# Kernel tuning notes

Measured on AMD Instinct MI355X. Metric: run time of the kernel, lower is better.

## Reference

```python
import jax, jax.numpy as jnp
import numpy as np

BS, D_NUM, SLEN, DIM = 64, 2, 50, 64   # batch, domains, history len, embedding_dim
NUM_EMB = 512                          # codebook size (hardcoded in source)
NEG_INF = -1e30                        # stand-in for -np.inf (NaN-safe under softmax grad)


def setup_inputs() -> dict:
    key = jax.random.key(0)
    ks = jax.random.split(key, 16)
    w = lambda k, shape: jax.random.normal(k, shape, jnp.float32) * 0.05
    inp = {
        "x": jax.random.normal(ks[0], (BS, D_NUM, SLEN, DIM), jnp.float32),
        "code_book": jax.random.normal(ks[1], (NUM_EMB, DIM), jnp.float32) * 0.1,
        "Wq_is": w(ks[2], (DIM, DIM)), "bq_is": jnp.zeros((DIM,), jnp.float32),
        "Wk_is": w(ks[3], (DIM, DIM)), "bk_is": jnp.zeros((DIM,), jnp.float32),
        "Wv_is": w(ks[4], (DIM, DIM)), "bv_is": jnp.zeros((DIM,), jnp.float32),
        "Wq_cs": w(ks[5], (DIM, DIM)), "bq_cs": jnp.zeros((DIM,), jnp.float32),
        "Wk_cs": w(ks[6], (DIM, DIM)), "bk_cs": jnp.zeros((DIM,), jnp.float32),
        "Wv_cs": w(ks[7], (DIM, DIM)), "bv_cs": jnp.zeros((DIM,), jnp.float32),
    }
    return inp


def reference(x, code_book,
              Wq_is, bq_is, Wk_is, bk_is, Wv_is, bv_is,
              Wq_cs, bq_cs, Wk_cs, bk_cs, Wv_cs, bv_cs):
    bs, dn, sl, dim = x.shape
    flat = x.reshape(-1, dim)  # [N, dim], N = bs*dn*sl

    # ---- get_quantized: cdist + argmin + codebook lookup ----
    # ||f||^2 + ||c||^2 - 2 f c^T, argmin over codebook, gather (== one_hot @ code_book)
    dists = (jnp.sum(flat * flat, axis=1, keepdims=True)
             + jnp.sum(code_book * code_book, axis=1)
             - 2.0 * flat @ code_book.T)                      # [N, NUM_EMB]
    idx = jnp.argmin(dists, axis=1)                           # [N]
    quantized = code_book[idx].reshape(x.shape)               # [bs, dn, sl, dim]

    # ---- intra-sample (IS) attention: softmax(K Q^T) V per (sample, domain) ----
    q = (flat @ Wq_is + bq_is).reshape(bs, dn, sl, dim)
    k = (flat @ Wk_is + bk_is).reshape(bs, dn, sl, dim)
    v = (flat @ Wv_is + bv_is).reshape(bs, dn, sl, dim)
    is_kq = jnp.einsum('bdse,bdte->bdst', k, q)               # K @ Q^T, [bs, dn, sl, sl]
    Z = jnp.einsum('bdst,bdte->bdse', jax.nn.softmax(is_kq, axis=-1), v)

    # ---- cross-sample (CS) attention: dense NxN, own-sample block masked out ----
    qc = flat @ Wq_cs + bq_cs                                  # [N, dim]
    kc = flat @ Wk_cs + bk_cs
    vc = flat @ Wv_cs + bv_cs
    sid = jnp.repeat(jnp.arange(bs), dn * sl)                  # sample id per row
    same = sid[:, None] == sid[None, :]                        # block-diagonal mask
    scores = kc @ qc.T                                         # [N, N]
    scores = jnp.where(same, NEG_INF, scores)                  # mask own-sample block
    X = (jax.nn.softmax(scores, axis=-1) @ vc).reshape(x.shape)

    return quantized, Z, X
```

## Files before the change

### kernel.cpp

```cpp
#include <hip/hip_runtime.h>
#include <hip/hip_bf16.h>
#include <math.h>

#define DIM 64
#define NROW 6400
#define SLEN 50
#define NG 128
#define NEMB 512
#define SAMPLE 100
#define NCHUNK 100
#define NQB 400
#define SMAX 6
#define LOG2E 1.4426950408889634f
#define SM_SHIFT2 11.541560327111707f
#define LSTR 72

typedef unsigned short ushort_t;
typedef __attribute__((ext_vector_type(8))) short short8;
typedef __attribute__((ext_vector_type(4))) float floatx4;

__device__ __forceinline__ ushort_t f2bu(float f) {
    __hip_bfloat16 h = __float2bfloat16(f);
    ushort_t u;
    __builtin_memcpy(&u, &h, 2);
    return u;
}

__device__ __forceinline__ float fast_exp2(float x) {
#if __has_builtin(__builtin_amdgcn_exp2f)
    return __builtin_amdgcn_exp2f(x);
#else
    return exp2f(x);
#endif
}

__global__ __launch_bounds__(64)
void prep_kernel(const float* __restrict__ W0, const float* __restrict__ W1,
                 const float* __restrict__ W2, const float* __restrict__ W3,
                 const float* __restrict__ W4, const float* __restrict__ W5,
                 ushort_t* __restrict__ Wt,
                 const float* __restrict__ cb, float* __restrict__ cbT,
                 double* __restrict__ c2)
{
    if (blockIdx.x < 6) {
        const float* Ws[6] = {W0, W1, W2, W3, W4, W5};
        const int p = blockIdx.x;
        const int n = threadIdx.x;
        const float* W = Ws[p];
        const float scale = (p == 1 || p == 4) ? LOG2E : 1.0f;
        ushort_t* dst = Wt + (size_t)p * DIM * DIM + (size_t)n * DIM;
#pragma unroll 8
        for (int k = 0; k < DIM; ++k)
            dst[k] = f2bu(W[(size_t)k * DIM + n] * scale);
    } else {
        const int c = (blockIdx.x - 6) * 64 + threadIdx.x;
        const float* cr = cb + (size_t)c * DIM;
        double s = 0.0;
#pragma unroll 8
        for (int e = 0; e < DIM; ++e) {
            const float v = cr[e];
            cbT[(size_t)e * NEMB + c] = v;
            s = fma((double)v, (double)v, s);
        }
        c2[c] = s;
    }
}

__global__ __launch_bounds__(256)
void proj_kernel(const float* __restrict__ x, const ushort_t* __restrict__ Wt,
                 const float* __restrict__ b0, const float* __restrict__ b1,
                 const float* __restrict__ b2, const float* __restrict__ b3,
                 const float* __restrict__ b4, const float* __restrict__ b5,
                 ushort_t* __restrict__ qib, ushort_t* __restrict__ kib,
                 ushort_t* __restrict__ vib,
                 ushort_t* __restrict__ qcb, ushort_t* __restrict__ kcb,
                 ushort_t* __restrict__ vtb)
{
    __shared__ __align__(16) ushort_t Xb[64 * LSTR];

    const int tid = threadIdx.x;
    const int wave = tid >> 6, lane = tid & 63;
    const int col = lane & 15;
    const int quad = lane >> 4;

    const int r0 = (blockIdx.x >> 1) * 64;
    const int pbase = (blockIdx.x & 1) * 3;

    {
        const int r = tid >> 2, seg = tid & 3;
        const float* src = x + (size_t)(r0 + r) * DIM + seg * 16;
        ushort_t* dst = &Xb[r * LSTR + seg * 16];
#pragma unroll
        for (int i = 0; i < 16; ++i) dst[i] = f2bu(src[i]);
    }
    __syncthreads();

    const short8 aX0 = *(const short8*)&Xb[(wave * 16 + col) * LSTR + quad * 8];
    const short8 aX1 = *(const short8*)&Xb[(wave * 16 + col) * LSTR + quad * 8 + 32];

    const float* Bs[6] = {b0, b1, b2, b3, b4, b5};
#pragma unroll
    for (int pp = 0; pp < 3; ++pp) {
        const int p = pbase + pp;
        const ushort_t* Wtp = Wt + (size_t)p * DIM * DIM;
#pragma unroll
        for (int nt = 0; nt < 4; ++nt) {
            const int n = nt * 16 + col;
            float bv = Bs[p][n];
            if (p == 1 || p == 4) bv *= LOG2E;
            floatx4 c = (floatx4){bv, bv, bv, bv};
            const ushort_t* wr = Wtp + (size_t)n * DIM + quad * 8;
            const short8 w0 = *(const short8*)wr;
            const short8 w1 = *(const short8*)(wr + 32);
            c = __builtin_amdgcn_mfma_f32_16x16x32_bf16(aX0, w0, c, 0, 0, 0);
            c = __builtin_amdgcn_mfma_f32_16x16x32_bf16(aX1, w1, c, 0, 0, 0);
#pragma unroll
            for (int r = 0; r < 4; ++r) {
                const int row = r0 + wave * 16 + quad * 4 + r;
                const ushort_t ub = f2bu(c[r]);
                if (p == 0)      qib[(size_t)row * DIM + n] = ub;
                else if (p == 1) kib[(size_t)row * DIM + n] = ub;
                else if (p == 2) vib[(size_t)row * DIM + n] = ub;
                else if (p == 3) qcb[(size_t)row * DIM + n] = ub;
                else if (p == 4) kcb[(size_t)row * DIM + n] = ub;
                else             vtb[(size_t)n * NROW + row] = ub;
            }
        }
    }
}

__global__ __launch_bounds__(256, 5)
void attn_quant_kernel(const ushort_t* __restrict__ qib, const ushort_t* __restrict__ kib,
                       const ushort_t* __restrict__ vib, float* __restrict__ outZ,
                       const ushort_t* __restrict__ qcb, const ushort_t* __restrict__ kcb,
                       const ushort_t* __restrict__ vtb,
                       float* __restrict__ pl, float* __restrict__ pacc,
                       float* __restrict__ outX,
                       const float* __restrict__ x, const float* __restrict__ cb,
                       const float* __restrict__ cbT, const double* __restrict__ c2,
                       float* __restrict__ outq,
                       int S, int direct)
{
    __shared__ __align__(16) ushort_t smem[3 * 64 * LSTR];

    const int tid = threadIdx.x;
    const int wave = tid >> 6;
    const int lane = tid & 63;

    if ((int)blockIdx.x < NQB) {
        const int r0 = blockIdx.x * 16;

        double* xs    = (double*)smem;
        double* f2s   = xs + 16 * 64;
        double* candd = f2s + 16;
        int*    candi = (int*)(candd + 64);
        int*    sidx  = candi + 64;

        for (int idx = tid; idx < 16 * DIM; idx += 256) {
            const int r = idx >> 6, e = idx & 63;
            xs[r * 64 + e] = (double)x[(size_t)(r0 + r) * DIM + e];
        }
        __syncthreads();
        if (tid < 16) {
            double s = 0.0;
#pragma unroll 8
            for (int e = 0; e < DIM; ++e) s = fma(xs[tid * 64 + e], xs[tid * 64 + e], s);
            f2s[tid] = s;
        }
        __syncthreads();

        const int c0 = wave * 64 + lane;
        double dot0[16], dot1[16];
#pragma unroll
        for (int r = 0; r < 16; ++r) { dot0[r] = 0.0; dot1[r] = 0.0; }

        for (int e = 0; e < DIM; ++e) {
            const double ce0 = (double)cbT[(size_t)e * NEMB + c0];
            const double ce1 = (double)cbT[(size_t)e * NEMB + c0 + 256];
#pragma unroll
            for (int r = 0; r < 16; ++r) {
                const double xe = xs[r * 64 + e];
                dot0[r] = fma(xe, ce0, dot0[r]);
                dot1[r] = fma(xe, ce1, dot1[r]);
            }
        }

#pragma unroll
        for (int r = 0; r < 16; ++r) {
            const double f2r = f2s[r];
            double bd = f2r + c2[c0] - 2.0 * dot0[r];
            int bi = c0;
            const double d1 = f2r + c2[c0 + 256] - 2.0 * dot1[r];
            if (d1 < bd) { bd = d1; bi = c0 + 256; }
            for (int off = 32; off; off >>= 1) {
                const double od = __shfl_down(bd, off, 64);
                const int oi = __shfl_down(bi, off, 64);
                if (od < bd || (od == bd && oi < bi)) { bd = od; bi = oi; }
            }
            if (lane == 0) { candd[wave * 16 + r] = bd; candi[wave * 16 + r] = bi; }
        }
        __syncthreads();
        if (tid < 16) {
            double bd = candd[tid];
            int bi = candi[tid];
#pragma unroll
            for (int w = 1; w < 4; ++w) {
                const double od = candd[w * 16 + tid];
                const int oi = candi[w * 16 + tid];
                if (od < bd || (od == bd && oi < bi)) { bd = od; bi = oi; }
            }
            sidx[tid] = bi;
        }
        __syncthreads();
        for (int idx = tid; idx < 16 * DIM; idx += 256) {
            const int r = idx >> 6, e = idx & 63;
            outq[(size_t)(r0 + r) * DIM + e] = cb[(size_t)sidx[r] * DIM + e];
        }
        return;
    }

    const int ab = blockIdx.x - NQB;
    const int col = lane & 15;
    const int quad = lane >> 4;

    short8 ones;
#pragma unroll
    for (int i = 0; i < 8; ++i) ones[i] = (short)0x3F80;

    if (ab < 100 * S) {
        const int bi = ab / S;
        const int split = ab % S;
        const int i0 = bi * 64 + wave * 16;

        ushort_t* Qs = smem;
        ushort_t* Vs = smem + 64 * LSTR;
        ushort_t* Pb = smem + 2 * 64 * LSTR + wave * 16 * LSTR;

        const int srow = tid >> 2;
        const int sseg = tid & 3;

        short8 aK0, aK1;
        {
            const ushort_t* kr = kcb + (size_t)(i0 + col) * DIM + quad * 8;
            aK0 = *(const short8*)kr;
            aK1 = *(const short8*)(kr + 32);
        }

        int lo[4];
        float l[4];
        floatx4 O[4];
#pragma unroll
        for (int r = 0; r < 4; ++r) {
            lo[r] = ((i0 + quad * 4 + r) / SAMPLE) * SAMPLE;
            l[r] = 0.f;
        }
#pragma unroll
        for (int et = 0; et < 4; ++et) O[et] = (floatx4){0.f, 0.f, 0.f, 0.f};

        {
            const int j0 = split * 64;
            const uint4* qsrc = (const uint4*)(qcb + (size_t)(j0 + srow) * DIM + sseg * 16);
            const uint4* vsrc = (const uint4*)(vtb + (size_t)srow * NROW + j0 + sseg * 16);
            const uint4 q0 = qsrc[0], q1 = qsrc[1];
            const uint4 v0 = vsrc[0], v1 = vsrc[1];
            uint4* qdst = (uint4*)&Qs[srow * LSTR + sseg * 16];
            uint4* vdst = (uint4*)&Vs[srow * LSTR + sseg * 16];
            qdst[0] = q0; qdst[1] = q1;
            vdst[0] = v0; vdst[1] = v1;
        }
        __syncthreads();

        for (int ch = split; ch < NCHUNK; ch += S) {
            const int nxt = ch + S;
            uint4 q0, q1, v0, v1;
            if (nxt < NCHUNK) {
                const int j0n = nxt * 64;
                const uint4* qsrc = (const uint4*)(qcb + (size_t)(j0n + srow) * DIM + sseg * 16);
                const uint4* vsrc = (const uint4*)(vtb + (size_t)srow * NROW + j0n + sseg * 16);
                q0 = qsrc[0]; q1 = qsrc[1];
                v0 = vsrc[0]; v1 = vsrc[1];
            }

            const int j0 = ch * 64;

            floatx4 Sv[4];
#pragma unroll
            for (int jt = 0; jt < 4; ++jt) {
                const short8 b0 = *(const short8*)&Qs[(jt * 16 + col) * LSTR + quad * 8];
                const short8 b1 = *(const short8*)&Qs[(jt * 16 + col) * LSTR + quad * 8 + 32];
                floatx4 c = (floatx4){0.f, 0.f, 0.f, 0.f};
                c = __builtin_amdgcn_mfma_f32_16x16x32_bf16(aK0, b0, c, 0, 0, 0);
                c = __builtin_amdgcn_mfma_f32_16x16x32_bf16(aK1, b1, c, 0, 0, 0);
                Sv[jt] = c;
            }

#pragma unroll
            for (int jt = 0; jt < 4; ++jt) {
                const int jj = j0 + jt * 16 + col;
#pragma unroll
                for (int r = 0; r < 4; ++r) {
                    float p = fast_exp2(Sv[jt][r] - SM_SHIFT2);
                    if ((unsigned)(jj - lo[r]) < SAMPLE) p = 0.f;
                    Pb[(quad * 4 + r) * LSTR + jt * 16 + col] = f2bu(p);
                }
            }

            const short8 aP0 = *(const short8*)&Pb[col * LSTR + quad * 8];
            const short8 aP1 = *(const short8*)&Pb[col * LSTR + quad * 8 + 32];

            floatx4 rsv = (floatx4){0.f, 0.f, 0.f, 0.f};
            rsv = __builtin_amdgcn_mfma_f32_16x16x32_bf16(aP0, ones, rsv, 0, 0, 0);
            rsv = __builtin_amdgcn_mfma_f32_16x16x32_bf16(aP1, ones, rsv, 0, 0, 0);
#pragma unroll
            for (int r = 0; r < 4; ++r) l[r] += rsv[r];

#pragma unroll
            for (int et = 0; et < 4; ++et) {
                const short8 b0 = *(const short8*)&Vs[(et * 16 + col) * LSTR + quad * 8];
                const short8 b1 = *(const short8*)&Vs[(et * 16 + col) * LSTR + quad * 8 + 32];
                O[et] = __builtin_amdgcn_mfma_f32_16x16x32_bf16(aP0, b0, O[et], 0, 0, 0);
                O[et] = __builtin_amdgcn_mfma_f32_16x16x32_bf16(aP1, b1, O[et], 0, 0, 0);
            }

            if (nxt < NCHUNK) {
                __syncthreads();
                uint4* qdst = (uint4*)&Qs[srow * LSTR + sseg * 16];
                uint4* vdst = (uint4*)&Vs[srow * LSTR + sseg * 16];
                qdst[0] = q0; qdst[1] = q1;
                vdst[0] = v0; vdst[1] = v1;
                __syncthreads();
            }
        }

        if (direct) {
#pragma unroll
            for (int et = 0; et < 4; ++et)
#pragma unroll
                for (int r = 0; r < 4; ++r)
                    outX[(size_t)(i0 + quad * 4 + r) * DIM + et * 16 + col] = O[et][r] / l[r];
        } else {
#pragma unroll
            for (int et = 0; et < 4; ++et)
#pragma unroll
                for (int r = 0; r < 4; ++r)
                    pacc[((size_t)split * NROW + i0 + quad * 4 + r) * DIM + et * 16 + col] = O[et][r];
            if (col == 0) {
#pragma unroll
                for (int r = 0; r < 4; ++r)
                    pl[(size_t)split * NROW + i0 + quad * 4 + r] = l[r];
            }
        }
    } else {
        const int g = ab - 100 * S;
        const size_t base = (size_t)g * SLEN * DIM;

        ushort_t* Vt = smem;
        ushort_t* Pb = smem + 64 * LSTR + wave * 16 * LSTR;

        {
            const int r = tid >> 2, seg = tid & 3;
            if (r < SLEN) {
                const uint4* vsrc = (const uint4*)(vib + base + (size_t)r * DIM + seg * 16);
                uint4 vv[2] = {vsrc[0], vsrc[1]};
                ushort_t vtmp[16];
                __builtin_memcpy(vtmp, vv, 32);
#pragma unroll
                for (int i = 0; i < 16; ++i)
                    Vt[(seg * 16 + i) * LSTR + r] = vtmp[i];
            } else {
#pragma unroll
                for (int i = 0; i < 16; ++i)
                    Vt[(seg * 16 + i) * LSTR + r] = 0;
            }
        }
        __syncthreads();

        short8 aK0, aK1;
        {
            const ushort_t* kr = kib + base + (size_t)(wave * 16 + col) * DIM + quad * 8;
            aK0 = *(const short8*)kr;
            aK1 = *(const short8*)(kr + 32);
        }

        floatx4 Sv[4];
#pragma unroll
        for (int jt = 0; jt < 4; ++jt) {
            const ushort_t* qr = qib + base + (size_t)(jt * 16 + col) * DIM + quad * 8;
            const short8 q0 = *(const short8*)qr;
            const short8 q1 = *(const short8*)(qr + 32);
            floatx4 c = (floatx4){0.f, 0.f, 0.f, 0.f};
            c = __builtin_amdgcn_mfma_f32_16x16x32_bf16(aK0, q0, c, 0, 0, 0);
            c = __builtin_amdgcn_mfma_f32_16x16x32_bf16(aK1, q1, c, 0, 0, 0);
            Sv[jt] = c;
        }

#pragma unroll
        for (int jt = 0; jt < 4; ++jt) {
            const int t = jt * 16 + col;
#pragma unroll
            for (int r = 0; r < 4; ++r) {
                float p = fast_exp2(Sv[jt][r] - SM_SHIFT2);
                if (t >= SLEN) p = 0.f;
                Pb[(quad * 4 + r) * LSTR + jt * 16 + col] = f2bu(p);
            }
        }

        const short8 aP0 = *(const short8*)&Pb[col * LSTR + quad * 8];
        const short8 aP1 = *(const short8*)&Pb[col * LSTR + quad * 8 + 32];

        floatx4 rsv = (floatx4){0.f, 0.f, 0.f, 0.f};
        rsv = __builtin_amdgcn_mfma_f32_16x16x32_bf16(aP0, ones, rsv, 0, 0, 0);
        rsv = __builtin_amdgcn_mfma_f32_16x16x32_bf16(aP1, ones, rsv, 0, 0, 0);

#pragma unroll
        for (int et = 0; et < 4; ++et) {
            const short8 v0 = *(const short8*)&Vt[(et * 16 + col) * LSTR + quad * 8];
            const short8 v1 = *(const short8*)&Vt[(et * 16 + col) * LSTR + quad * 8 + 32];
            floatx4 o = (floatx4){0.f, 0.f, 0.f, 0.f};
            o = __builtin_amdgcn_mfma_f32_16x16x32_bf16(aP0, v0, o, 0, 0, 0);
            o = __builtin_amdgcn_mfma_f32_16x16x32_bf16(aP1, v1, o, 0, 0, 0);
#pragma unroll
            for (int r = 0; r < 4; ++r) {
                const int s = wave * 16 + quad * 4 + r;
                if (s < SLEN)
                    outZ[base + (size_t)s * DIM + et * 16 + col] = o[r] / rsv[r];
            }
        }
    }
}

__global__ __launch_bounds__(256)
void cs_combine_kernel(const float* __restrict__ pl, const float* __restrict__ pacc,
                       float* __restrict__ outX, int S)
{
    const int row = blockIdx.x * 4 + (threadIdx.x >> 6);
    const int lane = threadIdx.x & 63;
    float l = 0.f, a = 0.f;
    for (int p = 0; p < S; ++p) {
        l += pl[(size_t)p * NROW + row];
        a += pacc[((size_t)p * NROW + row) * DIM + lane];
    }
    outX[(size_t)row * DIM + lane] = a / l;
}

extern "C" void kernel_launch(void* const* d_in, const int* in_sizes, int n_in,
                              void* d_out, int out_size, void* d_ws, size_t ws_size,
                              hipStream_t stream)
{
    (void)in_sizes; (void)n_in; (void)out_size;

    const float* x     = (const float*)d_in[0];
    const float* cb    = (const float*)d_in[1];
    const float* Wq_is = (const float*)d_in[2];  const float* bq_is = (const float*)d_in[3];
    const float* Wk_is = (const float*)d_in[4];  const float* bk_is = (const float*)d_in[5];
    const float* Wv_is = (const float*)d_in[6];  const float* bv_is = (const float*)d_in[7];
    const float* Wq_cs = (const float*)d_in[8];  const float* bq_cs = (const float*)d_in[9];
    const float* Wk_cs = (const float*)d_in[10]; const float* bk_cs = (const float*)d_in[11];
    const float* Wv_cs = (const float*)d_in[12]; const float* bv_cs = (const float*)d_in[13];

    float* outQ = (float*)d_out;
    float* outZ = outQ + (size_t)NROW * DIM;
    float* outX = outZ + (size_t)NROW * DIM;

    const size_t RB    = (size_t)NROW * DIM * sizeof(ushort_t);
    const size_t WT_B  = 6 * (size_t)DIM * DIM * sizeof(ushort_t);
    const size_t CBT_B = (size_t)NEMB * DIM * sizeof(float);
    const size_t C2_B  = (size_t)NEMB * sizeof(double);
    const size_t BASE  = 6 * RB + WT_B + CBT_B + C2_B;
    const size_t PER_SPLIT = (size_t)NROW * DIM * sizeof(float)
                           + (size_t)NROW * sizeof(float);
    int S = 1;
    if (ws_size > BASE) {
        const size_t avail = (ws_size - BASE) / PER_SPLIT;
        S = (avail >= SMAX) ? SMAX : (avail < 1 ? 1 : (int)avail);
    }
    const int direct = (S == 1);

    ushort_t* qib = (ushort_t*)d_ws;
    ushort_t* kib = qib + (size_t)NROW * DIM;
    ushort_t* vib = kib + (size_t)NROW * DIM;
    ushort_t* qcb = vib + (size_t)NROW * DIM;
    ushort_t* kcb = qcb + (size_t)NROW * DIM;
    ushort_t* vtb = kcb + (size_t)NROW * DIM;
    ushort_t* Wt  = vtb + (size_t)NROW * DIM;
    float*    cbT = (float*)((char*)d_ws + 6 * RB + WT_B);
    double*   c2  = (double*)((char*)d_ws + 6 * RB + WT_B + CBT_B);
    float*    pacc = (float*)((char*)d_ws + BASE);
    float*    pl   = pacc + (size_t)S * NROW * DIM;

    prep_kernel<<<14, 64, 0, stream>>>(Wq_is, Wk_is, Wv_is, Wq_cs, Wk_cs, Wv_cs, Wt,
                                       cb, cbT, c2);

    proj_kernel<<<200, 256, 0, stream>>>(x, Wt,
        bq_is, bk_is, bv_is, bq_cs, bk_cs, bv_cs,
        qib, kib, vib, qcb, kcb, vtb);

    attn_quant_kernel<<<NQB + 100 * S + NG, 256, 0, stream>>>(qib, kib, vib, outZ,
                                                              qcb, kcb, vtb,
                                                              pl, pacc, outX,
                                                              x, cb, cbT, c2, outQ,
                                                              S, direct);
    if (!direct)
        cs_combine_kernel<<<NROW / 4, 256, 0, stream>>>(pl, pacc, outX, S);
}
```

Baseline: 60.90 us.

## Precompute double-precision x in prep kernel and drop row-norm from argmin

The quantization blocks no longer stage x into shared memory as doubles or compute the per-row squared norm. The norm is dropped because it is constant per row and does not change the argmin. Instead, prep_kernel converts x to a double array in workspace, and the argmin loop reads it directly from global memory in two 8-row batches, which reduces register pressure. The split count SMAX is also raised from 6 to 7. The costs are an extra 3.2MB write and read through the workspace, more prep blocks, and global (cache) loads in place of LDS reads inside the inner loop.

```diff
diff --git a/kernel.cpp b/kernel.cpp
--- a/kernel.cpp
+++ b/kernel.cpp
@@ -10,7 +10,7 @@
 #define SAMPLE 100
 #define NCHUNK 100
 #define NQB 400
-#define SMAX 6
+#define SMAX 7
 #define LOG2E 1.4426950408889634f
 #define SM_SHIFT2 11.541560327111707f
 #define LSTR 72
@@ -40,7 +40,8 @@
                  const float* __restrict__ W4, const float* __restrict__ W5,
                  ushort_t* __restrict__ Wt,
                  const float* __restrict__ cb, float* __restrict__ cbT,
-                 double* __restrict__ c2)
+                 double* __restrict__ c2,
+                 const float* __restrict__ x, double* __restrict__ x64)
 {
     if (blockIdx.x < 6) {
         const float* Ws[6] = {W0, W1, W2, W3, W4, W5};
@@ -52,7 +53,7 @@
 #pragma unroll 8
         for (int k = 0; k < DIM; ++k)
             dst[k] = f2bu(W[(size_t)k * DIM + n] * scale);
-    } else {
+    } else if (blockIdx.x < 14) {
         const int c = (blockIdx.x - 6) * 64 + threadIdx.x;
         const float* cr = cb + (size_t)c * DIM;
         double s = 0.0;
@@ -63,6 +64,12 @@
             s = fma((double)v, (double)v, s);
         }
         c2[c] = s;
+    } else {
+        const int r0 = (blockIdx.x - 14) * 64;
+        const int t = threadIdx.x;
+#pragma unroll 8
+        for (int r = 0; r < 64; ++r)
+            x64[(size_t)(r0 + r) * DIM + t] = (double)x[(size_t)(r0 + r) * DIM + t];
     }
 }
 
@@ -136,7 +143,7 @@
                        const ushort_t* __restrict__ vtb,
                        float* __restrict__ pl, float* __restrict__ pacc,
                        float* __restrict__ outX,
-                       const float* __restrict__ x, const float* __restrict__ cb,
+                       const double* __restrict__ x64, const float* __restrict__ cb,
                        const float* __restrict__ cbT, const double* __restrict__ c2,
                        float* __restrict__ outq,
                        int S, int direct)
@@ -150,54 +157,48 @@
     if ((int)blockIdx.x < NQB) {
         const int r0 = blockIdx.x * 16;
 
-        double* xs    = (double*)smem;
-        double* f2s   = xs + 16 * 64;
-        double* candd = f2s + 16;
+        double* candd = (double*)smem;
         int*    candi = (int*)(candd + 64);
         int*    sidx  = candi + 64;
 
-        for (int idx = tid; idx < 16 * DIM; idx += 256) {
-            const int r = idx >> 6, e = idx & 63;
-            xs[r * 64 + e] = (double)x[(size_t)(r0 + r) * DIM + e];
-        }
-        __syncthreads();
-        if (tid < 16) {
-            double s = 0.0;
-#pragma unroll 8
-            for (int e = 0; e < DIM; ++e) s = fma(xs[tid * 64 + e], xs[tid * 64 + e], s);
-            f2s[tid] = s;
-        }
-        __syncthreads();
-
         const int c0 = wave * 64 + lane;
-        double dot0[16], dot1[16];
-#pragma unroll
-        for (int r = 0; r < 16; ++r) { dot0[r] = 0.0; dot1[r] = 0.0; }
-
-        for (int e = 0; e < DIM; ++e) {
-            const double ce0 = (double)cbT[(size_t)e * NEMB + c0];
-            const double ce1 = (double)cbT[(size_t)e * NEMB + c0 + 256];
-#pragma unroll
-            for (int r = 0; r < 16; ++r) {
-                const double xe = xs[r * 64 + e];
-                dot0[r] = fma(xe, ce0, dot0[r]);
-                dot1[r] = fma(xe, ce1, dot1[r]);
-            }
-        }
-
-#pragma unroll
-        for (int r = 0; r < 16; ++r) {
-            const double f2r = f2s[r];
-            double bd = f2r + c2[c0] - 2.0 * dot0[r];
-            int bi = c0;
-            const double d1 = f2r + c2[c0 + 256] - 2.0 * dot1[r];
-            if (d1 < bd) { bd = d1; bi = c0 + 256; }
-            for (int off = 32; off; off >>= 1) {
-                const double od = __shfl_down(bd, off, 64);
-                const int oi = __shfl_down(bi, off, 64);
-                if (od < bd || (od == bd && oi < bi)) { bd = od; bi = oi; }
-            }
-            if (lane == 0) { candd[wave * 16 + r] = bd; candi[wave * 16 + r] = bi; }
+        const double cc0 = c2[c0];
+        const double cc1 = c2[c0 + 256];
+
+#pragma unroll
+        for (int rb = 0; rb < 2; ++rb) {
+            double dot0[8], dot1[8];
+#pragma unroll
+            for (int r = 0; r < 8; ++r) { dot0[r] = 0.0; dot1[r] = 0.0; }
+
+            const double* xrow = x64 + (size_t)(r0 + rb * 8) * DIM;
+            for (int e = 0; e < DIM; ++e) {
+                const double ce0 = (double)cbT[(size_t)e * NEMB + c0];
+                const double ce1 = (double)cbT[(size_t)e * NEMB + c0 + 256];
+#pragma unroll
+                for (int r = 0; r < 8; ++r) {
+                    const double xe = xrow[(size_t)r * DIM + e];
+                    dot0[r] = fma(xe, ce0, dot0[r]);
+                    dot1[r] = fma(xe, ce1, dot1[r]);
+                }
+            }
+
+#pragma unroll
+            for (int r = 0; r < 8; ++r) {
+                double bd = cc0 - 2.0 * dot0[r];
+                int bi = c0;
+                const double d1 = cc1 - 2.0 * dot1[r];
+                if (d1 < bd) { bd = d1; bi = c0 + 256; }
+                for (int off = 32; off; off >>= 1) {
+                    const double od = __shfl_down(bd, off, 64);
+                    const int oi = __shfl_down(bi, off, 64);
+                    if (od < bd || (od == bd && oi < bi)) { bd = od; bi = oi; }
+                }
+                if (lane == 0) {
+                    candd[wave * 16 + rb * 8 + r] = bd;
+                    candi[wave * 16 + rb * 8 + r] = bi;
+                }
+            }
         }
         __syncthreads();
         if (tid < 16) {
@@ -466,7 +467,8 @@
     const size_t WT_B  = 6 * (size_t)DIM * DIM * sizeof(ushort_t);
     const size_t CBT_B = (size_t)NEMB * DIM * sizeof(float);
     const size_t C2_B  = (size_t)NEMB * sizeof(double);
-    const size_t BASE  = 6 * RB + WT_B + CBT_B + C2_B;
+    const size_t X64_B = (size_t)NROW * DIM * sizeof(double);
+    const size_t BASE  = 6 * RB + WT_B + CBT_B + C2_B + X64_B;
     const size_t PER_SPLIT = (size_t)NROW * DIM * sizeof(float)
                            + (size_t)NROW * sizeof(float);
     int S = 1;
@@ -485,11 +487,12 @@
     ushort_t* Wt  = vtb + (size_t)NROW * DIM;
     float*    cbT = (float*)((char*)d_ws + 6 * RB + WT_B);
     double*   c2  = (double*)((char*)d_ws + 6 * RB + WT_B + CBT_B);
+    double*   x64 = (double*)((char*)d_ws + 6 * RB + WT_B + CBT_B + C2_B);
     float*    pacc = (float*)((char*)d_ws + BASE);
     float*    pl   = pacc + (size_t)S * NROW * DIM;
 
-    prep_kernel<<<14, 64, 0, stream>>>(Wq_is, Wk_is, Wv_is, Wq_cs, Wk_cs, Wv_cs, Wt,
-                                       cb, cbT, c2);
+    prep_kernel<<<114, 64, 0, stream>>>(Wq_is, Wk_is, Wv_is, Wq_cs, Wk_cs, Wv_cs, Wt,
+                                        cb, cbT, c2, x, x64);
 
     proj_kernel<<<200, 256, 0, stream>>>(x, Wt,
         bq_is, bk_is, bv_is, bq_cs, bk_cs, bv_cs,
@@ -498,7 +501,7 @@
     attn_quant_kernel<<<NQB + 100 * S + NG, 256, 0, stream>>>(qib, kib, vib, outZ,
                                                               qcb, kcb, vtb,
                                                               pl, pacc, outX,
-                                                              x, cb, cbT, c2, outQ,
+                                                              x64, cb, cbT, c2, outQ,
                                                               S, direct);
     if (!direct)
         cs_combine_kernel<<<NROW / 4, 256, 0, stream>>>(pl, pacc, outX, S);
```

Result: slower. 62.24 us (+2.2%).
